# Kernel optimization log

Hardware: AMD Instinct MI355X
Metric: run time of the kernel (lower is better)

## Reference

```python
import jax, jax.numpy as jnp
import numpy as np

E = 100          # number of elements
K = 4            # codes per element (core set = all elements)
C = E * K        # total codes
D = 128          # embed_dim
N = 262144       # atoms in batch
GAMMA = 0.99     # ema_decay
BETA = 0.25      # commitment_weight


def setup_inputs() -> dict:
    key = jax.random.key(0)
    k1, k2, k3, k4 = jax.random.split(key, 4)
    h = jax.random.normal(k1, (N, D), dtype=jnp.float32)
    elem_indices = jax.random.randint(k2, (N,), 0, E, dtype=jnp.int32)
    codebook = jax.random.normal(k3, (C, D), dtype=jnp.float32)
    ema_count = jax.random.uniform(k4, (C,), dtype=jnp.float32, minval=0.5, maxval=2.0)
    ema_embed_sum = codebook * ema_count[:, None]
    return {"h": h, "elem_indices": elem_indices, "codebook": codebook,
            "ema_count": ema_count, "ema_embed_sum": ema_embed_sum}


def reference(h, elem_indices, codebook, ema_count, ema_embed_sum):
    # element id owning each code (uniform contiguous ranges of size K)
    code_elem = jnp.repeat(jnp.arange(E, dtype=elem_indices.dtype), K)  # [C]

    # masked cdist (euclidean): ||h||^2 + ||c||^2 - 2 h.c, inf outside own range
    d2 = (jnp.sum(h * h, axis=1, keepdims=True)
          + jnp.sum(codebook * codebook, axis=1)[None, :]
          - 2.0 * h @ codebook.T)                                # [N, C]
    dist = jnp.sqrt(jnp.maximum(d2, 0.0))
    valid = jnp.where(code_elem[None, :] == elem_indices[:, None], dist, jnp.inf)

    atom_types = jnp.argmin(valid, axis=1)                       # [N]
    z_q = codebook[atom_types]                                   # [N, D]
    h_q = h + jax.lax.stop_gradient(z_q - h)                     # straight-through

    # all elements are multi-code -> commitment over every atom
    commitment_loss = jnp.mean((h - jax.lax.stop_gradient(z_q)) ** 2)
    vq_loss = BETA * commitment_loss

    # EMA codebook update (training path, no_grad in original)
    counts = jax.ops.segment_sum(jnp.ones((N,), h.dtype), atom_types, num_segments=C)  # [C]
    sums = jax.ops.segment_sum(h, atom_types, num_segments=C)                          # [C, D]
    elem_present = jax.ops.segment_sum(jnp.ones((N,), h.dtype), elem_indices,
                                       num_segments=E) > 0                              # [E]
    code_present = jnp.repeat(elem_present, K)                                          # [C]

    new_count = jnp.where(code_present, GAMMA * ema_count + (1.0 - GAMMA) * counts, ema_count)
    new_sum = jnp.where(code_present[:, None],
                        GAMMA * ema_embed_sum + (1.0 - GAMMA) * sums, ema_embed_sum)
    new_codebook = jnp.where(code_present[:, None],
                             new_sum / jnp.maximum(new_count, 1e-5)[:, None], codebook)

    return h_q, atom_types, vq_loss, new_codebook, new_count, new_sum
```

## Files before the change

### kernel.cpp

```cpp
#include <hip/hip_runtime.h>
#include <hip/hip_bf16.h>

#define D_ 128
#define E_ 100
#define K_ 4
#define C_ 400
#define NCHUNK 128
#define SCALE 65536.0f
#define INV_SCALE (1.0f / 65536.0f)

#define OFF_COUNTS 51200
#define OFF_LOSS   51600
#define OFF_PSUM   51712
#define PSUM_SZ    (256 * C_ * 64)
#define OFF_PCNT   (OFF_PSUM + PSUM_SZ)
#define WS_NEED_PART ((size_t)(OFF_PCNT + NCHUNK * C_) * 4)

template <int CTRL>
__device__ __forceinline__ float dpp_add(float x) {
  int y = __builtin_amdgcn_update_dpp(0, __builtin_bit_cast(int, x),
                                      CTRL, 0xF, 0xF, true);
  return x + __builtin_bit_cast(float, y);
}

__device__ __forceinline__ float dist8(float4 hA, float4 hB, float4 cA, float4 cB) {
  float d0 = hA.x - cA.x, d1 = hA.y - cA.y;
  float d2 = hA.z - cA.z, d3 = hA.w - cA.w;
  float d4 = hB.x - cB.x, d5 = hB.y - cB.y;
  float d6 = hB.z - cB.z, d7 = hB.w - cB.w;
  return ((d0*d0 + d1*d1) + (d2*d2 + d3*d3)) +
         ((d4*d4 + d5*d5) + (d6*d6 + d7*d7));
}

__global__ __launch_bounds__(256) void k_assign(
    const float* __restrict__ h, const int* __restrict__ ei,
    const float* __restrict__ cb, float* __restrict__ hq,
    float* __restrict__ at, float* __restrict__ loss_acc, int N) {
  const int lane16 = threadIdx.x & 15;
  const int gid = (blockIdx.x * 256 + threadIdx.x) >> 4;
  const int ngroups = (gridDim.x * 256) >> 4;
  const float4* h4 = (const float4*)h;
  const float4* cb4 = (const float4*)cb;
  float4* hq4 = (float4*)hq;
  float loss = 0.f;

  int a = gid;
  bool ok = a < N;
  int as = ok ? a : 0;
  int e = ei[as];
  float4 hA = h4[(size_t)as * 32 + lane16 * 2];
  float4 hB = h4[(size_t)as * 32 + lane16 * 2 + 1];

  while (ok) {
    const int an = a + ngroups;
    const bool okn = an < N;
    const int ans = okn ? an : a;
    const int en = ei[ans];
    const float4 hAn = h4[(size_t)ans * 32 + lane16 * 2];
    const float4 hBn = h4[(size_t)ans * 32 + lane16 * 2 + 1];

    const size_t cb0 = (size_t)e * (K_ * 32) + lane16 * 2;
    float4 cA0 = cb4[cb0],      cB0 = cb4[cb0 + 1];
    float4 cA1 = cb4[cb0 + 32], cB1 = cb4[cb0 + 33];
    float4 cA2 = cb4[cb0 + 64], cB2 = cb4[cb0 + 65];
    float4 cA3 = cb4[cb0 + 96], cB3 = cb4[cb0 + 97];

    float p0 = dist8(hA, hB, cA0, cB0);
    float p1 = dist8(hA, hB, cA1, cB1);
    float p2 = dist8(hA, hB, cA2, cB2);
    float p3 = dist8(hA, hB, cA3, cB3);

    p0 = dpp_add<0xB1>(p0); p1 = dpp_add<0xB1>(p1);
    p2 = dpp_add<0xB1>(p2); p3 = dpp_add<0xB1>(p3);
    p0 = dpp_add<0x4E>(p0); p1 = dpp_add<0x4E>(p1);
    p2 = dpp_add<0x4E>(p2); p3 = dpp_add<0x4E>(p3);
    p0 = dpp_add<0x141>(p0); p1 = dpp_add<0x141>(p1);
    p2 = dpp_add<0x141>(p2); p3 = dpp_add<0x141>(p3);
    p0 = dpp_add<0x140>(p0); p1 = dpp_add<0x140>(p1);
    p2 = dpp_add<0x140>(p2); p3 = dpp_add<0x140>(p3);

    int best = 0; float bp = p0;
    if (p1 < bp) { bp = p1; best = 1; }
    if (p2 < bp) { bp = p2; best = 2; }
    if (p3 < bp) { bp = p3; best = 3; }

    float4 qA = cA0, qB = cB0;
    if (best == 1) { qA = cA1; qB = cB1; }
    if (best == 2) { qA = cA2; qB = cB2; }
    if (best == 3) { qA = cA3; qB = cB3; }
    hq4[(size_t)a * 32 + lane16 * 2]     = qA;
    hq4[(size_t)a * 32 + lane16 * 2 + 1] = qB;
    if (lane16 == 0) {
      at[a] = (float)(e * K_ + best);
      loss += bp;
    }

    a = an; ok = okn; e = en; hA = hAn; hB = hBn;
  }

  loss += __shfl_xor(loss, 16, 64);
  loss += __shfl_xor(loss, 32, 64);
  __shared__ float wl[4];
  const int w = threadIdx.x >> 6;
  if ((threadIdx.x & 63) == 0) wl[w] = loss;
  __syncthreads();
  if (threadIdx.x == 0)
    atomicAdd(loss_acc, wl[0] + wl[1] + wl[2] + wl[3]);
}

__global__ __launch_bounds__(1024) void k_sums3(
    const float* __restrict__ h, const float* __restrict__ at,
    int* __restrict__ psumI, int* __restrict__ pcntI,
    float* __restrict__ sums, float* __restrict__ countsF,
    int dopart, int N) {
  const int half = blockIdx.x & 1;
  const int chunk = blockIdx.x >> 1;
  __shared__ int acc[C_ * 64];
  __shared__ int cnt[C_];
  for (int i = threadIdx.x; i < C_ * 64; i += 1024) acc[i] = 0;
  if (half == 0)
    for (int i = threadIdx.x; i < C_; i += 1024) cnt[i] = 0;
  __syncthreads();

  const int per = (N + NCHUNK - 1) / NCHUNK;
  const int a0 = chunk * per;
  const int aEnd = min(a0 + per, N);
  const int w = threadIdx.x >> 6;
  const int lane = threadIdx.x & 63;
  const int g = lane >> 4, t = lane & 15;
  const float4* h4 = (const float4*)h;

  int a = a0 + w * 4 + g;
  bool ok0 = a < aEnd, ok1 = (a + 64) < aEnd;
  float4 v0 = {}, v1 = {}; int c0 = 0, c1 = 0;
  if (ok0) { v0 = h4[(size_t)a * 32 + half * 16 + t]; c0 = (int)at[a]; }
  if (ok1) { v1 = h4[(size_t)(a + 64) * 32 + half * 16 + t]; c1 = (int)at[a + 64]; }

  while (ok0) {
    const int an = a + 128;
    const bool okn = an < aEnd;
    float4 vn = {}; int cn = 0;
    if (okn) { vn = h4[(size_t)an * 32 + half * 16 + t]; cn = (int)at[an]; }

    int* ap = &acc[c0 * 64 + t * 4];
    int iv0 = __float2int_rn(v0.x * SCALE);
    int iv1 = __float2int_rn(v0.y * SCALE);
    int iv2 = __float2int_rn(v0.z * SCALE);
    int iv3 = __float2int_rn(v0.w * SCALE);
    if (g == 0) { atomicAdd(&ap[0],iv0); atomicAdd(&ap[1],iv1); atomicAdd(&ap[2],iv2); atomicAdd(&ap[3],iv3); }
    else if (g == 1) { atomicAdd(&ap[1],iv1); atomicAdd(&ap[2],iv2); atomicAdd(&ap[3],iv3); atomicAdd(&ap[0],iv0); }
    else if (g == 2) { atomicAdd(&ap[2],iv2); atomicAdd(&ap[3],iv3); atomicAdd(&ap[0],iv0); atomicAdd(&ap[1],iv1); }
    else { atomicAdd(&ap[3],iv3); atomicAdd(&ap[0],iv0); atomicAdd(&ap[1],iv1); atomicAdd(&ap[2],iv2); }
    if (half == 0 && t == 0) atomicAdd(&cnt[c0], 1);

    a += 64;
    ok0 = ok1; v0 = v1; c0 = c1;
    ok1 = okn; v1 = vn; c1 = cn;
  }
  __syncthreads();

  if (dopart) {
    int* pb = psumI + (size_t)blockIdx.x * (C_ * 64);
    for (int i = threadIdx.x; i < C_ * 64; i += 1024) pb[i] = acc[i];
    if (half == 0) {
      int* pc = pcntI + (size_t)chunk * C_;
      for (int i = threadIdx.x; i < C_; i += 1024) pc[i] = cnt[i];
    }
  } else {
    for (int i = threadIdx.x; i < C_ * 64; i += 1024) {
      int vv = acc[i];
      if (vv != 0)
        atomicAdd(&sums[(size_t)(i >> 6) * D_ + half * 64 + (i & 63)],
                  (float)vv * INV_SCALE);
    }
    if (half == 0)
      for (int i = threadIdx.x; i < C_; i += 1024)
        if (cnt[i] != 0) atomicAdd(&countsF[i], (float)cnt[i]);
  }
}

__global__ __launch_bounds__(256) void k_reduce(
    const int* __restrict__ psumI, const int* __restrict__ pcntI,
    float* __restrict__ sums, float* __restrict__ countsF) {
  int idx = blockIdx.x * 256 + threadIdx.x;
  if (idx < C_ * D_) {
    int code = idx >> 7;
    int dim = idx & 127;
    int half = dim >> 6;
    int dl = dim & 63;
    const int* p = psumI + (size_t)half * (C_ * 64) + code * 64 + dl;
    float s = 0.f;
    for (int b = 0; b < NCHUNK; ++b)
      s += (float)p[(size_t)b * 2 * (C_ * 64)];
    sums[idx] = s * INV_SCALE;
  }
  if (idx < C_) {
    int s = 0;
    for (int b = 0; b < NCHUNK; ++b)
      s += pcntI[(size_t)b * C_ + idx];
    countsF[idx] = (float)s;
  }
}

__global__ __launch_bounds__(256) void k_final(
    const float* __restrict__ cb, const float* __restrict__ ecnt,
    const float* __restrict__ esum, const float* __restrict__ ws,
    float* __restrict__ out, int N) {
  const float* sums = ws;
  const float* countsF = ws + OFF_COUNTS;
  int idx = blockIdx.x * 256 + threadIdx.x;
  const size_t base = (size_t)N * D_ + N + 1;
  if (idx < C_ * D_) {
    int c = idx >> 7;
    int e4 = (c >> 2) << 2;
    bool present = (countsF[e4] + countsF[e4 + 1] + countsF[e4 + 2] + countsF[e4 + 3]) > 0.f;
    float es = esum[idx];
    float s  = sums[idx];
    float ns = present ? 0.99f * es + 0.01f * s : es;
    float ec = ecnt[c];
    float nc = present ? 0.99f * ec + 0.01f * countsF[c] : ec;
    float ncbv = present ? ns / fmaxf(nc, 1e-5f) : cb[idx];
    out[base + idx] = ncbv;
    if ((idx & 127) == 0) out[base + C_ * D_ + c] = nc;
    out[base + C_ * D_ + C_ + idx] = ns;
  }
  if (idx == 0) {
    float loss = ws[OFF_LOSS];
    out[(size_t)N * D_ + N] = 0.25f * loss / ((float)N * (float)D_);
  }
}

extern "C" void kernel_launch(void* const* d_in, const int* in_sizes, int n_in,
                              void* d_out, int out_size, void* d_ws, size_t ws_size,
                              hipStream_t stream) {
  const float* h = nullptr; const int* ei = nullptr;
  const float* cb = nullptr; const float* ecnt = nullptr; const float* esum = nullptr;
  long hsz = -1; int hidx = -1;
  for (int i = 0; i < n_in; ++i)
    if ((long)in_sizes[i] > hsz) { hsz = in_sizes[i]; hidx = i; }
  h = (const float*)d_in[hidx];
  const int N = (int)(hsz / D_);
  for (int i = 0; i < n_in; ++i) {
    if (i == hidx) continue;
    const int s = in_sizes[i];
    if (s == N) ei = (const int*)d_in[i];
    else if (s == C_) ecnt = (const float*)d_in[i];
    else if (s == C_ * D_) { if (!cb) cb = (const float*)d_in[i]; else esum = (const float*)d_in[i]; }
  }

  float* out = (float*)d_out;
  float* hq  = out;
  float* at  = out + (size_t)N * D_;

  float* ws = (float*)d_ws;
  float* sums    = ws;
  float* countsF = ws + OFF_COUNTS;
  float* lossp   = ws + OFF_LOSS;
  int*   psumI   = (int*)(ws + OFF_PSUM);
  int*   pcntI   = (int*)(ws + OFF_PCNT);

  const int dopart = (ws_size >= WS_NEED_PART) ? 1 : 0;

  hipMemsetAsync(d_ws, 0, (size_t)(OFF_LOSS + 1) * 4, stream);

  k_assign<<<2048, 256, 0, stream>>>(h, ei, cb, hq, at, lossp, N);
  k_sums3<<<NCHUNK * 2, 1024, 0, stream>>>(h, at, psumI, pcntI,
                                           sums, countsF, dopart, N);
  if (dopart)
    k_reduce<<<(C_ * D_ + 255) / 256, 256, 0, stream>>>(psumI, pcntI, sums, countsF);
  k_final<<<(C_ * D_ + 255) / 256, 256, 0, stream>>>(cb, ecnt, esum, ws, out, N);
}
```

Before: 112.8 us.

## Stage codebook halves in LDS and split assignment into two element-range passes

The assignment kernel now copies half of the codebook (50 elements, 200 rows, padded to 33 float4 per row) into shared memory and is launched twice, each launch handling only the atoms whose element falls in its half. Codebook reads move from global/L1 gathers to padded LDS reads, and blocks grow to 1024 threads. In exchange, every launch scans the whole index array, each atom's row is read only by the pass that owns it, the software prefetch of h is removed, and a second launch adds overhead. The roughly 103 KB LDS footprint limits occupancy to one block per CU.

```diff
diff --git a/kernel.cpp b/kernel.cpp
--- a/kernel.cpp
+++ b/kernel.cpp
@@ -32,80 +32,85 @@
          ((d4*d4 + d5*d5) + (d6*d6 + d7*d7));
 }
 
-__global__ __launch_bounds__(256) void k_assign(
+__global__ __launch_bounds__(1024) void k_asg(
     const float* __restrict__ h, const int* __restrict__ ei,
     const float* __restrict__ cb, float* __restrict__ hq,
-    float* __restrict__ at, float* __restrict__ loss_acc, int N) {
-  const int lane16 = threadIdx.x & 15;
-  const int gid = (blockIdx.x * 256 + threadIdx.x) >> 4;
-  const int ngroups = (gridDim.x * 256) >> 4;
+    float* __restrict__ at, float* __restrict__ loss_acc,
+    int N, int elo, int ehi) {
+  __shared__ float4 cbl[200 * 33];
+  __shared__ float wl[16];
+  const int tid = threadIdx.x;
+  const float4* cb4 = (const float4*)cb;
+  const int nrow = (ehi - elo) * K_;
+  for (int idx = tid; idx < nrow * 32; idx += 1024) {
+    int r = idx >> 5, k = idx & 31;
+    cbl[r * 33 + k] = cb4[(size_t)(elo * K_ + r) * 32 + k];
+  }
+  __syncthreads();
+
+  const int t = tid & 15;
+  const int gid = blockIdx.x * 64 + (tid >> 4);
+  const int ngroups = gridDim.x * 64;
   const float4* h4 = (const float4*)h;
-  const float4* cb4 = (const float4*)cb;
   float4* hq4 = (float4*)hq;
   float loss = 0.f;
 
-  int a = gid;
-  bool ok = a < N;
-  int as = ok ? a : 0;
-  int e = ei[as];
-  float4 hA = h4[(size_t)as * 32 + lane16 * 2];
-  float4 hB = h4[(size_t)as * 32 + lane16 * 2 + 1];
-
-  while (ok) {
+  int e = ei[gid < N ? gid : 0];
+  for (int a = gid; a < N; a += ngroups) {
     const int an = a + ngroups;
-    const bool okn = an < N;
-    const int ans = okn ? an : a;
-    const int en = ei[ans];
-    const float4 hAn = h4[(size_t)ans * 32 + lane16 * 2];
-    const float4 hBn = h4[(size_t)ans * 32 + lane16 * 2 + 1];
-
-    const size_t cb0 = (size_t)e * (K_ * 32) + lane16 * 2;
-    float4 cA0 = cb4[cb0],      cB0 = cb4[cb0 + 1];
-    float4 cA1 = cb4[cb0 + 32], cB1 = cb4[cb0 + 33];
-    float4 cA2 = cb4[cb0 + 64], cB2 = cb4[cb0 + 65];
-    float4 cA3 = cb4[cb0 + 96], cB3 = cb4[cb0 + 97];
-
-    float p0 = dist8(hA, hB, cA0, cB0);
-    float p1 = dist8(hA, hB, cA1, cB1);
-    float p2 = dist8(hA, hB, cA2, cB2);
-    float p3 = dist8(hA, hB, cA3, cB3);
-
-    p0 = dpp_add<0xB1>(p0); p1 = dpp_add<0xB1>(p1);
-    p2 = dpp_add<0xB1>(p2); p3 = dpp_add<0xB1>(p3);
-    p0 = dpp_add<0x4E>(p0); p1 = dpp_add<0x4E>(p1);
-    p2 = dpp_add<0x4E>(p2); p3 = dpp_add<0x4E>(p3);
-    p0 = dpp_add<0x141>(p0); p1 = dpp_add<0x141>(p1);
-    p2 = dpp_add<0x141>(p2); p3 = dpp_add<0x141>(p3);
-    p0 = dpp_add<0x140>(p0); p1 = dpp_add<0x140>(p1);
-    p2 = dpp_add<0x140>(p2); p3 = dpp_add<0x140>(p3);
-
-    int best = 0; float bp = p0;
-    if (p1 < bp) { bp = p1; best = 1; }
-    if (p2 < bp) { bp = p2; best = 2; }
-    if (p3 < bp) { bp = p3; best = 3; }
-
-    float4 qA = cA0, qB = cB0;
-    if (best == 1) { qA = cA1; qB = cB1; }
-    if (best == 2) { qA = cA2; qB = cB2; }
-    if (best == 3) { qA = cA3; qB = cB3; }
-    hq4[(size_t)a * 32 + lane16 * 2]     = qA;
-    hq4[(size_t)a * 32 + lane16 * 2 + 1] = qB;
-    if (lane16 == 0) {
-      at[a] = (float)(e * K_ + best);
-      loss += bp;
+    const int en = ei[an < N ? an : a];
+    if (e >= elo && e < ehi) {
+      float4 hA = h4[(size_t)a * 32 + t * 2];
+      float4 hB = h4[(size_t)a * 32 + t * 2 + 1];
+      const int r0 = (e - elo) * K_;
+      float4 cA0 = cbl[(r0+0)*33 + t*2], cB0 = cbl[(r0+0)*33 + t*2 + 1];
+      float4 cA1 = cbl[(r0+1)*33 + t*2], cB1 = cbl[(r0+1)*33 + t*2 + 1];
+      float4 cA2 = cbl[(r0+2)*33 + t*2], cB2 = cbl[(r0+2)*33 + t*2 + 1];
+      float4 cA3 = cbl[(r0+3)*33 + t*2], cB3 = cbl[(r0+3)*33 + t*2 + 1];
+
+      float p0 = dist8(hA, hB, cA0, cB0);
+      float p1 = dist8(hA, hB, cA1, cB1);
+      float p2 = dist8(hA, hB, cA2, cB2);
+      float p3 = dist8(hA, hB, cA3, cB3);
+
+      p0 = dpp_add<0xB1>(p0); p1 = dpp_add<0xB1>(p1);
+      p2 = dpp_add<0xB1>(p2); p3 = dpp_add<0xB1>(p3);
+      p0 = dpp_add<0x4E>(p0); p1 = dpp_add<0x4E>(p1);
+      p2 = dpp_add<0x4E>(p2); p3 = dpp_add<0x4E>(p3);
+      p0 = dpp_add<0x141>(p0); p1 = dpp_add<0x141>(p1);
+      p2 = dpp_add<0x141>(p2); p3 = dpp_add<0x141>(p3);
+      p0 = dpp_add<0x140>(p0); p1 = dpp_add<0x140>(p1);
+      p2 = dpp_add<0x140>(p2); p3 = dpp_add<0x140>(p3);
+
+      int best = 0; float bp = p0;
+      if (p1 < bp) { bp = p1; best = 1; }
+      if (p2 < bp) { bp = p2; best = 2; }
+      if (p3 < bp) { bp = p3; best = 3; }
+
+      float4 qA = cA0, qB = cB0;
+      if (best == 1) { qA = cA1; qB = cB1; }
+      if (best == 2) { qA = cA2; qB = cB2; }
+      if (best == 3) { qA = cA3; qB = cB3; }
+      hq4[(size_t)a * 32 + t * 2]     = qA;
+      hq4[(size_t)a * 32 + t * 2 + 1] = qB;
+      if (t == 0) {
+        at[a] = (float)(e * K_ + best);
+        loss += bp;
+      }
     }
-
-    a = an; ok = okn; e = en; hA = hAn; hB = hBn;
+    e = en;
   }
 
   loss += __shfl_xor(loss, 16, 64);
   loss += __shfl_xor(loss, 32, 64);
-  __shared__ float wl[4];
-  const int w = threadIdx.x >> 6;
-  if ((threadIdx.x & 63) == 0) wl[w] = loss;
-  __syncthreads();
-  if (threadIdx.x == 0)
-    atomicAdd(loss_acc, wl[0] + wl[1] + wl[2] + wl[3]);
+  if ((tid & 63) == 0) wl[tid >> 6] = loss;
+  __syncthreads();
+  if (tid == 0) {
+    float s = 0.f;
+#pragma unroll
+    for (int i = 0; i < 16; ++i) s += wl[i];
+    atomicAdd(loss_acc, s);
+  }
 }
 
 __global__ __launch_bounds__(1024) void k_sums3(
@@ -263,7 +268,8 @@
 
   hipMemsetAsync(d_ws, 0, (size_t)(OFF_LOSS + 1) * 4, stream);
 
-  k_assign<<<2048, 256, 0, stream>>>(h, ei, cb, hq, at, lossp, N);
+  k_asg<<<256, 1024, 0, stream>>>(h, ei, cb, hq, at, lossp, N, 0, E_ / 2);
+  k_asg<<<256, 1024, 0, stream>>>(h, ei, cb, hq, at, lossp, N, E_ / 2, E_);
   k_sums3<<<NCHUNK * 2, 1024, 0, stream>>>(h, at, psumI, pcntI,
                                            sums, countsF, dopart, N);
   if (dopart)
```

Measured after the change: 116.9 us. +3.6%, slower.
